# Kernel tuning notes

Hardware: AMD Instinct MI355X
Metric: run time of the kernel (lower is better)

## Reference

```python
import jax, jax.numpy as jnp
import numpy as np

N = 4096
IN_DIM = 256
HID = 64
NHEADS = 4
OUT_DIM = 128
ALPHA = 0.5  # LeakyReLU negative slope
NEG_INF = -9e15


def gat_layer(x, mask, W, a, concat):
    """Dense GraphAttentionLayer (pyGAT style).
    x:[N,Fin], mask:[N,N] bool, W:[Fin,Fout], a:[2*Fout]."""
    Wh = x @ W                                   # [N, Fout]
    Fout = W.shape[1]
    f1 = Wh @ a[:Fout]                           # [N]
    f2 = Wh @ a[Fout:]                           # [N]
    e = jax.nn.leaky_relu(f1[:, None] + f2[None, :], negative_slope=ALPHA)  # [N,N]
    att = jax.nn.softmax(jnp.where(mask, e, NEG_INF), axis=1)               # [N,N]
    h = att @ Wh                                 # [N, Fout]
    return jax.nn.elu(h) if concat else h


def setup_inputs() -> dict:
    key = jax.random.key(0)
    ks = jax.random.split(key, 6)
    x = jax.random.normal(ks[0], (N, IN_DIM), dtype=jnp.float32)
    adj = jax.random.randint(ks[1], (N, N), 0, 2, dtype=jnp.int32)
    s_in = 1.0 / np.sqrt(IN_DIM)
    s_hid = 1.0 / np.sqrt(HID * NHEADS)
    W_heads = jax.random.uniform(ks[2], (NHEADS, IN_DIM, HID), jnp.float32, -s_in, s_in)
    a_heads = jax.random.uniform(ks[3], (NHEADS, 2 * HID), jnp.float32, -s_in, s_in)
    W_out = jax.random.uniform(ks[4], (HID * NHEADS, OUT_DIM), jnp.float32, -s_hid, s_hid)
    a_out = jax.random.uniform(ks[5], (2 * OUT_DIM,), jnp.float32, -s_hid, s_hid)
    return {"x": x, "adj": adj, "W_heads": W_heads, "a_heads": a_heads,
            "W_out": W_out, "a_out": a_out}


def reference(x, adj, W_heads, a_heads, W_out, a_out):
    mask = adj > 0
    # multi-head attention, concat along feature dim
    heads = jax.vmap(lambda W, a: gat_layer(x, mask, W, a, True))(W_heads, a_heads)
    h = jnp.transpose(heads, (1, 0, 2)).reshape(N, NHEADS * HID)  # [N, H*HID]
    # dropout=0 -> identity; final GAT layer (concat=False) + outer ELU
    out = jax.nn.elu(gat_layer(h, mask, W_out, a_out, False))     # [N, OUT_DIM]
    return out
```

## Files before the change

### kernel.cpp

```cpp
#include <hip/hip_runtime.h>
#include <hip/hip_bf16.h>

#define N 4096
#define IN_DIM 256
#define HID 64
#define NHEADS 4
#define OUT_DIM 128
#define LOG2E 1.44269504088896340736f

typedef __attribute__((ext_vector_type(8))) short bf16x8;
typedef __attribute__((ext_vector_type(4))) float f32x4;

__device__ __forceinline__ ushort2 bsplit(float v) {
    const ushort h = __hip_bfloat16_raw(__float2bfloat16(v)).x;
    const float vh = __uint_as_float((unsigned)h << 16);
    const ushort l = __hip_bfloat16_raw(__float2bfloat16(v - vh)).x;
    return make_ushort2(h, l);
}

__global__ __launch_bounds__(256, 4) void prep_kernel(
        const float* __restrict__ x, const float* __restrict__ W,
        const float* __restrict__ a, const int* __restrict__ adj,
        __hip_bfloat16* __restrict__ WhB,
        float* __restrict__ E1, float* __restrict__ S1,
        float* __restrict__ E2, float* __restrict__ S2,
        unsigned* __restrict__ maskT) {
    const int t = threadIdx.x;
    if (blockIdx.x < 256) {
        const int h = t >> 6, lane = t & 63, m = lane & 15, quad = lane >> 4;
        const int i0 = blockIdx.x * 16;
        const float* xrow = x + (size_t)(i0 + m) * IN_DIM;
        const float* Wp = W + (size_t)h * IN_DIM * HID;
        const f32x4 zero = {0.f, 0.f, 0.f, 0.f};
        f32x4 acc[4] = {zero, zero, zero, zero};
        for (int ks = 0; ks < 8; ks++) {
            const int kb = ks * 32 + quad * 8;
            const float4 xa = *(const float4*)(xrow + kb);
            const float4 xb = *(const float4*)(xrow + kb + 4);
            const float xf[8] = {xa.x, xa.y, xa.z, xa.w, xb.x, xb.y, xb.z, xb.w};
            bf16x8 xh, xl;
#pragma unroll
            for (int e = 0; e < 8; e++) {
                const ushort2 s = bsplit(xf[e]);
                xh[e] = (short)s.x; xl[e] = (short)s.y;
            }
#pragma unroll
            for (int ct = 0; ct < 4; ct++) {
                bf16x8 wh, wl;
#pragma unroll
                for (int e = 0; e < 8; e++) {
                    const ushort2 s =
                        bsplit(Wp[(size_t)(kb + e) * HID + ct * 16 + m]);
                    wh[e] = (short)s.x; wl[e] = (short)s.y;
                }
                acc[ct] = __builtin_amdgcn_mfma_f32_16x16x32_bf16(
                    xh, wh, acc[ct], 0, 0, 0);
                acc[ct] = __builtin_amdgcn_mfma_f32_16x16x32_bf16(
                    xl, wh, acc[ct], 0, 0, 0);
                acc[ct] = __builtin_amdgcn_mfma_f32_16x16x32_bf16(
                    xh, wl, acc[ct], 0, 0, 0);
            }
        }
        const int jblk = i0 >> 5, jb2 = (i0 >> 4) & 1;
#pragma unroll
        for (int ct = 0; ct < 4; ct++) {
#pragma unroll
            for (int r = 0; r < 4; r++) {
                const int jo = quad * 4 + r;
                const int lane_idx = m + 16 * (2 * jb2 + (jo >> 3));
                WhB[((((size_t)h * (N / 32) + jblk) * 4 + ct) * 64 + lane_idx) *
                        8 + (jo & 7)] = __float2bfloat16(acc[ct][r]);
            }
        }
        float av1[4], av2[4];
#pragma unroll
        for (int ct = 0; ct < 4; ct++) {
            av1[ct] = a[h * 2 * HID + ct * 16 + m];
            av2[ct] = a[h * 2 * HID + HID + ct * 16 + m];
        }
        float s1[4], s2[4];
#pragma unroll
        for (int r = 0; r < 4; r++) {
            s1[r] = 0.f; s2[r] = 0.f;
#pragma unroll
            for (int ct = 0; ct < 4; ct++) {
                s1[r] += acc[ct][r] * av1[ct];
                s2[r] += acc[ct][r] * av2[ct];
            }
        }
#pragma unroll
        for (int mm = 8; mm > 0; mm >>= 1) {
#pragma unroll
            for (int r = 0; r < 4; r++) {
                s1[r] += __shfl_xor(s1[r], mm, 64);
                s2[r] += __shfl_xor(s2[r], mm, 64);
            }
        }
        if (m == 0) {
#pragma unroll
            for (int r = 0; r < 4; r++) {
                const size_t ix = (size_t)h * N + i0 + quad * 4 + r;
                E1[ix] = __builtin_amdgcn_exp2f(s1[r] * LOG2E);
                S1[ix] = __builtin_amdgcn_exp2f(s1[r] * (0.5f * LOG2E));
                E2[ix] = __builtin_amdgcn_exp2f(s2[r] * LOG2E);
                S2[ix] = __builtin_amdgcn_exp2f(s2[r] * (0.5f * LOG2E));
            }
        }
    } else {
        const int lane = t & 63, w = t >> 6;
        const int i = (blockIdx.x - 256) * 4 + w;
        const int4* arow = (const int4*)(adj + (size_t)i * N);
        for (int jb = 0; jb < N / 256; jb++) {
            const int4 a4 = arow[jb * 64 + lane];
            unsigned long long bal[4];
            bal[0] = __ballot(a4.x > 0);
            bal[1] = __ballot(a4.y > 0);
            bal[2] = __ballot(a4.z > 0);
            bal[3] = __ballot(a4.w > 0);
            if (lane < 8) {
                unsigned word = 0;
#pragma unroll
                for (int e = 0; e < 4; e++) {
                    unsigned xv = (unsigned)(bal[e] >> (8 * lane)) & 0xFFu;
                    xv = (xv | (xv << 12)) & 0x000F000Fu;
                    xv = (xv | (xv << 6))  & 0x03030303u;
                    xv = (xv | (xv << 3))  & 0x11111111u;
                    word |= xv << e;
                }
                maskT[(size_t)(jb * 8 + lane) * N + i] = word;
            }
        }
    }
}

template <int HEADS, int D, int DSL, int G, int MW, int OCC>
__global__ __launch_bounds__(G * 64, OCC) void attn_fused(
        const unsigned* __restrict__ maskT,
        const __hip_bfloat16* __restrict__ WhB,
        const float* __restrict__ E1g, const float* __restrict__ S1g,
        const float* __restrict__ E2g, const float* __restrict__ S2g,
        float* __restrict__ outp) {
    constexpr int CTtot = D / 16;
    constexpr int CTT = CTtot / DSL;
    constexpr int CC = (D == 64) ? 1 : 2;
    constexpr int KSTEPS = N / (32 * G);
    __shared__ float sh[MW * G * 16 * CC * 17];
    __shared__ float dsh[MW * G * 16];
    const int t = threadIdx.x;
    const int g = t >> 6, lane = t & 63;
    const int m = lane & 15, quad = lane >> 4;
    const int h = blockIdx.y / DSL, slc = blockIdx.y % DSL;
    const int i0 = blockIdx.x * (16 * MW);

    float e1v[MW], s1v[MW];
#pragma unroll
    for (int mw = 0; mw < MW; mw++) {
        e1v[mw] = E1g[(size_t)h * N + i0 + mw * 16 + m];
        s1v[mw] = S1g[(size_t)h * N + i0 + mw * 16 + m];
    }

    const unsigned* mp = maskT + (size_t)(g * KSTEPS) * N + i0 + m;
    const float* ep = E2g + (size_t)h * N + g * (N / G) + quad * 8;
    const float* sp = S2g + (size_t)h * N + g * (N / G) + quad * 8;
    const bf16x8* bp = (const bf16x8*)WhB +
                       ((size_t)h * (N / 32) * CTtot +
                        (size_t)(g * KSTEPS) * CTtot + slc * CTT) * 64 + lane;

    const f32x4 zero = {0.f, 0.f, 0.f, 0.f};
    f32x4 acc[MW][CTT];
    f32x4 sac[MW];
#pragma unroll
    for (int mw = 0; mw < MW; mw++) {
        sac[mw] = zero;
#pragma unroll
        for (int ct = 0; ct < CTT; ct++) acc[mw][ct] = zero;
    }
    const short one_bf = (short)0x3F80;
    const bf16x8 ones = {one_bf, one_bf, one_bf, one_bf,
                         one_bf, one_bf, one_bf, one_bf};

    unsigned mwrd[2][MW];
    float4 e2lo[2], e2hi[2], s2lo[2], s2hi[2];
    auto stage = [&](int b) {
#pragma unroll
        for (int mw = 0; mw < MW; mw++) mwrd[b][mw] = mp[mw * 16];
        e2lo[b] = *(const float4*)(ep);
        e2hi[b] = *(const float4*)(ep + 4);
        s2lo[b] = *(const float4*)(sp);
        s2hi[b] = *(const float4*)(sp + 4);
    };

    stage(0); mp += N; ep += 32; sp += 32;
#pragma unroll 2
    for (int ks = 0; ks < KSTEPS; ks++) {
        const int cur = ks & 1;
        bf16x8 bfrag[CTT];
#pragma unroll
        for (int ct = 0; ct < CTT; ct++) bfrag[ct] = bp[ct * 64];
        bp += CTtot * 64;
        if (ks + 1 < KSTEPS) { stage(cur ^ 1); mp += N; ep += 32; sp += 32; }
        const float Ee[8] = {e2lo[cur].x, e2lo[cur].y, e2lo[cur].z, e2lo[cur].w,
                             e2hi[cur].x, e2hi[cur].y, e2hi[cur].z, e2hi[cur].w};
        const float Se[8] = {s2lo[cur].x, s2lo[cur].y, s2lo[cur].z, s2lo[cur].w,
                             s2hi[cur].x, s2hi[cur].y, s2hi[cur].z, s2hi[cur].w};
        bf16x8 afr[MW];
#pragma unroll
        for (int mw = 0; mw < MW; mw++) {
            const unsigned mword = (mwrd[cur][mw] >> (quad * 8)) & 0xFFu;
            const unsigned spread = mword * 0x8001u;
            float p[8];
#pragma unroll
            for (int e = 0; e < 8; e++)
                p[e] = fmaxf(e1v[mw] * Ee[e], s1v[mw] * Se[e]);
            union { bf16x8 v; unsigned u32[4]; __hip_bfloat162 h2[4]; } u;
#pragma unroll
            for (int e2 = 0; e2 < 4; e2++) {
                u.h2[e2] = __float22bfloat162_rn(
                    make_float2(p[2 * e2], p[2 * e2 + 1]));
                const unsigned mk =
                    ((spread >> (2 * e2)) & 0x00010001u) * 0xFFFFu;
                u.u32[e2] &= mk;
            }
            afr[mw] = u.v;
        }
#pragma unroll
        for (int ct = 0; ct < CTT; ct++)
#pragma unroll
            for (int mw = 0; mw < MW; mw++)
                acc[mw][ct] = __builtin_amdgcn_mfma_f32_16x16x32_bf16(
                    afr[mw], bfrag[ct], acc[mw][ct], 0, 0, 0);
#pragma unroll
        for (int mw = 0; mw < MW; mw++)
            sac[mw] = __builtin_amdgcn_mfma_f32_16x16x32_bf16(
                afr[mw], ones, sac[mw], 0, 0, 0);
    }

#pragma unroll
    for (int rd = 0; rd < CTT / CC; rd++) {
#pragma unroll
        for (int mw = 0; mw < MW; mw++) {
#pragma unroll
            for (int cc = 0; cc < CC; cc++) {
#pragma unroll
                for (int r = 0; r < 4; r++)
                    sh[(((mw * G + g) * 16 + quad * 4 + r) * CC + cc) * 17 + m] =
                        acc[mw][rd * CC + cc][r];
            }
            if (rd == 0 && m == 0) {
#pragma unroll
                for (int r = 0; r < 4; r++)
                    dsh[(mw * G + g) * 16 + quad * 4 + r] = sac[mw][r];
            }
        }
        __syncthreads();
        if (t < 16 * CC * 16) {
            int row, chl;
            if (D == 64) { row = t & 15; chl = (t >> 4) & 15; }
            else         { chl = t & 31; row = (t >> 5) & 15; }
#pragma unroll
            for (int mw = 0; mw < MW; mw++) {
                float av = 0.f, ss = 0.f;
#pragma unroll
                for (int gg = 0; gg < G; gg++) {
                    av += sh[(((mw * G + gg) * 16 + row) * CC + (chl >> 4)) * 17 +
                             (chl & 15)];
                    ss += dsh[(mw * G + gg) * 16 + row];
                }
                float v = av / ss;
                v = (v > 0.f) ? v : (__builtin_amdgcn_exp2f(v * LOG2E) - 1.f);
                const int chg = h * D + slc * (CTT * 16) + rd * CC * 16 + chl;
                const int irow = i0 + mw * 16 + row;
                if (D == 64)
                    outp[(size_t)irow * (NHEADS * HID) + chg] = v;
                else
                    outp[(size_t)irow * D + chg] = v;
            }
        }
        __syncthreads();
    }
}

__global__ __launch_bounds__(512, 2) void gemm2_kernel(
        const float* __restrict__ h1, const float* __restrict__ W2,
        const float* __restrict__ a2, __hip_bfloat16* __restrict__ WhB2,
        float* __restrict__ E1, float* __restrict__ S1,
        float* __restrict__ E2, float* __restrict__ S2) {
    __shared__ float fred[8][16][2];
    const int t = threadIdx.x;
    const int w = t >> 6, lane = t & 63, m = lane & 15, quad = lane >> 4;
    const int i0 = blockIdx.x * 16;
    const float* arow = h1 + (size_t)(i0 + m) * IN_DIM;
    const float* wp = W2 + w * 16 + m;
    const f32x4 zero = {0.f, 0.f, 0.f, 0.f};
    f32x4 acc = zero;
    for (int ks = 0; ks < 8; ks++) {
        const int kb = ks * 32 + quad * 8;
        const float4 xa = *(const float4*)(arow + kb);
        const float4 xb = *(const float4*)(arow + kb + 4);
        const float xf[8] = {xa.x, xa.y, xa.z, xa.w, xb.x, xb.y, xb.z, xb.w};
        bf16x8 xh, xl, wh, wl;
#pragma unroll
        for (int e = 0; e < 8; e++) {
            const ushort2 s = bsplit(xf[e]);
            xh[e] = (short)s.x; xl[e] = (short)s.y;
        }
#pragma unroll
        for (int e = 0; e < 8; e++) {
            const ushort2 s = bsplit(wp[(size_t)(kb + e) * OUT_DIM]);
            wh[e] = (short)s.x; wl[e] = (short)s.y;
        }
        acc = __builtin_amdgcn_mfma_f32_16x16x32_bf16(xh, wh, acc, 0, 0, 0);
        acc = __builtin_amdgcn_mfma_f32_16x16x32_bf16(xl, wh, acc, 0, 0, 0);
        acc = __builtin_amdgcn_mfma_f32_16x16x32_bf16(xh, wl, acc, 0, 0, 0);
    }
    const int jblk = i0 >> 5, jb2 = (i0 >> 4) & 1;
#pragma unroll
    for (int r = 0; r < 4; r++) {
        const int jo = quad * 4 + r;
        const int lane_idx = m + 16 * (2 * jb2 + (jo >> 3));
        WhB2[(((size_t)jblk * 8 + w) * 64 + lane_idx) * 8 + (jo & 7)] =
            __float2bfloat16(acc[r]);
    }
    const float av1 = a2[w * 16 + m], av2 = a2[OUT_DIM + w * 16 + m];
    float s1[4], s2[4];
#pragma unroll
    for (int r = 0; r < 4; r++) { s1[r] = acc[r] * av1; s2[r] = acc[r] * av2; }
#pragma unroll
    for (int mm = 8; mm > 0; mm >>= 1) {
#pragma unroll
        for (int r = 0; r < 4; r++) {
            s1[r] += __shfl_xor(s1[r], mm, 64);
            s2[r] += __shfl_xor(s2[r], mm, 64);
        }
    }
    if (m == 0) {
#pragma unroll
        for (int r = 0; r < 4; r++) {
            fred[w][quad * 4 + r][0] = s1[r];
            fred[w][quad * 4 + r][1] = s2[r];
        }
    }
    __syncthreads();
    if (t < 32) {
        const int row = t & 15, fn = t >> 4;
        float s = 0.f;
#pragma unroll
        for (int w8 = 0; w8 < 8; w8++) s += fred[w8][row][fn];
        const float e = __builtin_amdgcn_exp2f(s * LOG2E);
        const float sq = __builtin_amdgcn_exp2f(s * (0.5f * LOG2E));
        if (fn) { E2[i0 + row] = e; S2[i0 + row] = sq; }
        else    { E1[i0 + row] = e; S1[i0 + row] = sq; }
    }
}

extern "C" void kernel_launch(void* const* d_in, const int* in_sizes, int n_in,
                              void* d_out, int out_size, void* d_ws, size_t ws_size,
                              hipStream_t stream) {
    const float* x   = (const float*)d_in[0];
    const int*   adj = (const int*)d_in[1];
    const float* Wh_ = (const float*)d_in[2];
    const float* ah  = (const float*)d_in[3];
    const float* W2  = (const float*)d_in[4];
    const float* a2  = (const float*)d_in[5];
    float* out = (float*)d_out;

    float* ws = (float*)d_ws;
    float* E1a = ws;
    float* S1a = E1a + (size_t)NHEADS * N;
    float* E2a = S1a + (size_t)NHEADS * N;
    float* S2a = E2a + (size_t)NHEADS * N;
    float* E1b = S2a + (size_t)NHEADS * N;
    float* S1b = E1b + N;
    float* E2b = S1b + N;
    float* S2b = E2b + N;
    float* h1  = S2b + N;
    __hip_bfloat16* WhB1 = (__hip_bfloat16*)(h1 + (size_t)IN_DIM * N);
    __hip_bfloat16* WhB2 = WhB1 + (size_t)NHEADS * HID * N;
    unsigned* maskT = (unsigned*)(WhB2 + (size_t)OUT_DIM * N);

    prep_kernel<<<1280, 256, 0, stream>>>(x, Wh_, ah, adj, WhB1,
                                          E1a, S1a, E2a, S2a, maskT);
    attn_fused<NHEADS, HID, 1, 8, 2, 2>
        <<<dim3(N / 32, NHEADS), 512, 0, stream>>>(maskT, WhB1,
                                                   E1a, S1a, E2a, S2a, h1);
    gemm2_kernel<<<N / 16, 512, 0, stream>>>(h1, W2, a2, WhB2,
                                             E1b, S1b, E2b, S2b);
    attn_fused<1, OUT_DIM, 1, 8, 1, 2>
        <<<dim3(N / 16, 1), 512, 0, stream>>>(maskT, WhB2,
                                              E1b, S1b, E2b, S2b, out);
}
```

Measured before the change: 168.7 us.

## Fuse four kernels into one persistent megakernel with software grid barriers

Merges prep, first attention, second GEMM and final attention into a single persistent kernel of 512 blocks, separated by atomic-counter grid barriers. A memset resets the barrier counters before each launch. The goal is to drop three kernel launch gaps and the tail idle time between stages. In exchange, correctness now relies on all 512 blocks being co-resident, and the spin barriers use a timeout break. The second attention stage also changes its tiling from one block per 16 rows with a full 128-column slice to two 64-column slices, so it fits the fixed grid.

```diff
diff --git a/kernel.cpp b/kernel.cpp
--- a/kernel.cpp
+++ b/kernel.cpp
@@ -7,6 +7,7 @@
 #define NHEADS 4
 #define OUT_DIM 128
 #define LOG2E 1.44269504088896340736f
+#define NBLK 512
 
 typedef __attribute__((ext_vector_type(8))) short bf16x8;
 typedef __attribute__((ext_vector_type(4))) float f32x4;
@@ -18,97 +19,188 @@
     return make_ushort2(h, l);
 }
 
-__global__ __launch_bounds__(256, 4) void prep_kernel(
+__device__ __forceinline__ void grid_sync(unsigned* cnt) {
+    __syncthreads();
+    if (threadIdx.x == 0) {
+        __threadfence();
+        __hip_atomic_fetch_add(cnt, 1u, __ATOMIC_RELAXED,
+                               __HIP_MEMORY_SCOPE_AGENT);
+        int spins = 0;
+        while (__hip_atomic_load(cnt, __ATOMIC_RELAXED,
+                                 __HIP_MEMORY_SCOPE_AGENT) < NBLK) {
+            __builtin_amdgcn_s_sleep(8);
+            if (++spins > (1 << 22)) break;
+        }
+        __threadfence();
+    }
+    __syncthreads();
+}
+
+template <int D, int DSL, int G, int MW>
+__device__ __forceinline__ void attn_stage(
+        const int bx, const int by,
+        const unsigned* __restrict__ maskT,
+        const __hip_bfloat16* __restrict__ WhB,
+        const float* __restrict__ E1g, const float* __restrict__ S1g,
+        const float* __restrict__ E2g, const float* __restrict__ S2g,
+        float* __restrict__ outp, float* __restrict__ sh,
+        float* __restrict__ dsh) {
+    constexpr int CTtot = D / 16;
+    constexpr int CTT = CTtot / DSL;
+    constexpr int CC = (D == 64) ? 1 : 2;
+    constexpr int KSTEPS = N / (32 * G);
+    const int t = threadIdx.x;
+    const int g = t >> 6, lane = t & 63;
+    const int m = lane & 15, quad = lane >> 4;
+    const int h = by / DSL, slc = by % DSL;
+    const int i0 = bx * (16 * MW);
+
+    float e1v[MW], s1v[MW];
+#pragma unroll
+    for (int mw = 0; mw < MW; mw++) {
+        e1v[mw] = E1g[(size_t)h * N + i0 + mw * 16 + m];
+        s1v[mw] = S1g[(size_t)h * N + i0 + mw * 16 + m];
+    }
+    const unsigned* mp = maskT + (size_t)(g * KSTEPS) * N + i0 + m;
+    const float* ep = E2g + (size_t)h * N + g * (N / G) + quad * 8;
+    const float* sp = S2g + (size_t)h * N + g * (N / G) + quad * 8;
+    const bf16x8* bp = (const bf16x8*)WhB +
+                       ((size_t)h * (N / 32) * CTtot +
+                        (size_t)(g * KSTEPS) * CTtot + slc * CTT) * 64 + lane;
+
+    const f32x4 zero = {0.f, 0.f, 0.f, 0.f};
+    f32x4 acc[MW][CTT];
+    f32x4 sac[MW];
+#pragma unroll
+    for (int mw = 0; mw < MW; mw++) {
+        sac[mw] = zero;
+#pragma unroll
+        for (int ct = 0; ct < CTT; ct++) acc[mw][ct] = zero;
+    }
+    const short one_bf = (short)0x3F80;
+    const bf16x8 ones = {one_bf, one_bf, one_bf, one_bf,
+                         one_bf, one_bf, one_bf, one_bf};
+
+    unsigned mwrd[2][MW];
+    float4 e2lo[2], e2hi[2], s2lo[2], s2hi[2];
+    auto stage = [&](int b) {
+#pragma unroll
+        for (int mw = 0; mw < MW; mw++) mwrd[b][mw] = mp[mw * 16];
+        e2lo[b] = *(const float4*)(ep);
+        e2hi[b] = *(const float4*)(ep + 4);
+        s2lo[b] = *(const float4*)(sp);
+        s2hi[b] = *(const float4*)(sp + 4);
+    };
+
+    stage(0); mp += N; ep += 32; sp += 32;
+#pragma unroll 2
+    for (int ks = 0; ks < KSTEPS; ks++) {
+        const int cur = ks & 1;
+        bf16x8 bfrag[CTT];
+#pragma unroll
+        for (int ct = 0; ct < CTT; ct++) bfrag[ct] = bp[ct * 64];
+        bp += CTtot * 64;
+        if (ks + 1 < KSTEPS) { stage(cur ^ 1); mp += N; ep += 32; sp += 32; }
+        const float Ee[8] = {e2lo[cur].x, e2lo[cur].y, e2lo[cur].z, e2lo[cur].w,
+                             e2hi[cur].x, e2hi[cur].y, e2hi[cur].z, e2hi[cur].w};
+        const float Se[8] = {s2lo[cur].x, s2lo[cur].y, s2lo[cur].z, s2lo[cur].w,
+                             s2hi[cur].x, s2hi[cur].y, s2hi[cur].z, s2hi[cur].w};
+        bf16x8 afr[MW];
+#pragma unroll
+        for (int mw = 0; mw < MW; mw++) {
+            const unsigned mword = (mwrd[cur][mw] >> (quad * 8)) & 0xFFu;
+            const unsigned spread = mword * 0x8001u;
+            float p[8];
+#pragma unroll
+            for (int e = 0; e < 8; e++)
+                p[e] = fmaxf(e1v[mw] * Ee[e], s1v[mw] * Se[e]);
+            union { bf16x8 v; unsigned u32[4]; __hip_bfloat162 h2[4]; } u;
+#pragma unroll
+            for (int e2 = 0; e2 < 4; e2++) {
+                u.h2[e2] = __float22bfloat162_rn(
+                    make_float2(p[2 * e2], p[2 * e2 + 1]));
+                const unsigned mk =
+                    ((spread >> (2 * e2)) & 0x00010001u) * 0xFFFFu;
+                u.u32[e2] &= mk;
+            }
+            afr[mw] = u.v;
+        }
+#pragma unroll
+        for (int ct = 0; ct < CTT; ct++)
+#pragma unroll
+            for (int mw = 0; mw < MW; mw++)
+                acc[mw][ct] = __builtin_amdgcn_mfma_f32_16x16x32_bf16(
+                    afr[mw], bfrag[ct], acc[mw][ct], 0, 0, 0);
+#pragma unroll
+        for (int mw = 0; mw < MW; mw++)
+            sac[mw] = __builtin_amdgcn_mfma_f32_16x16x32_bf16(
+                afr[mw], ones, sac[mw], 0, 0, 0);
+    }
+
+#pragma unroll
+    for (int rd = 0; rd < CTT / CC; rd++) {
+#pragma unroll
+        for (int mw = 0; mw < MW; mw++) {
+#pragma unroll
+            for (int cc = 0; cc < CC; cc++) {
+#pragma unroll
+                for (int r = 0; r < 4; r++)
+                    sh[(((mw * G + g) * 16 + quad * 4 + r) * CC + cc) * 17 + m] =
+                        acc[mw][rd * CC + cc][r];
+            }
+            if (rd == 0 && m == 0) {
+#pragma unroll
+                for (int r = 0; r < 4; r++)
+                    dsh[(mw * G + g) * 16 + quad * 4 + r] = sac[mw][r];
+            }
+        }
+        __syncthreads();
+        if (t < 16 * CC * 16) {
+            int row, chl;
+            if (D == 64) { row = t & 15; chl = (t >> 4) & 15; }
+            else         { chl = t & 31; row = (t >> 5) & 15; }
+#pragma unroll
+            for (int mw = 0; mw < MW; mw++) {
+                float av = 0.f, ss = 0.f;
+#pragma unroll
+                for (int gg = 0; gg < G; gg++) {
+                    av += sh[(((mw * G + gg) * 16 + row) * CC + (chl >> 4)) * 17 +
+                             (chl & 15)];
+                    ss += dsh[(mw * G + gg) * 16 + row];
+                }
+                float v = av / ss;
+                v = (v > 0.f) ? v : (__builtin_amdgcn_exp2f(v * LOG2E) - 1.f);
+                const int chg = h * D + slc * (CTT * 16) + rd * CC * 16 + chl;
+                const int irow = i0 + mw * 16 + row;
+                if (D == 64)
+                    outp[(size_t)irow * (NHEADS * HID) + chg] = v;
+                else
+                    outp[(size_t)irow * D + chg] = v;
+            }
+        }
+        __syncthreads();
+    }
+}
+
+__global__ __launch_bounds__(512, 4) void mega(
         const float* __restrict__ x, const float* __restrict__ W,
         const float* __restrict__ a, const int* __restrict__ adj,
-        __hip_bfloat16* __restrict__ WhB,
-        float* __restrict__ E1, float* __restrict__ S1,
-        float* __restrict__ E2, float* __restrict__ S2,
-        unsigned* __restrict__ maskT) {
+        const float* __restrict__ W2, const float* __restrict__ a2,
+        __hip_bfloat16* __restrict__ WhB1, __hip_bfloat16* __restrict__ WhB2,
+        float* __restrict__ E1a, float* __restrict__ S1a,
+        float* __restrict__ E2a, float* __restrict__ S2a,
+        float* __restrict__ E1b, float* __restrict__ S1b,
+        float* __restrict__ E2b, float* __restrict__ S2b,
+        float* __restrict__ h1, unsigned* __restrict__ maskT,
+        float* __restrict__ out, unsigned* __restrict__ bars) {
+    __shared__ float shbuf[4608];
+    __shared__ float dshbuf[256];
     const int t = threadIdx.x;
-    if (blockIdx.x < 256) {
-        const int h = t >> 6, lane = t & 63, m = lane & 15, quad = lane >> 4;
-        const int i0 = blockIdx.x * 16;
-        const float* xrow = x + (size_t)(i0 + m) * IN_DIM;
-        const float* Wp = W + (size_t)h * IN_DIM * HID;
-        const f32x4 zero = {0.f, 0.f, 0.f, 0.f};
-        f32x4 acc[4] = {zero, zero, zero, zero};
-        for (int ks = 0; ks < 8; ks++) {
-            const int kb = ks * 32 + quad * 8;
-            const float4 xa = *(const float4*)(xrow + kb);
-            const float4 xb = *(const float4*)(xrow + kb + 4);
-            const float xf[8] = {xa.x, xa.y, xa.z, xa.w, xb.x, xb.y, xb.z, xb.w};
-            bf16x8 xh, xl;
-#pragma unroll
-            for (int e = 0; e < 8; e++) {
-                const ushort2 s = bsplit(xf[e]);
-                xh[e] = (short)s.x; xl[e] = (short)s.y;
-            }
-#pragma unroll
-            for (int ct = 0; ct < 4; ct++) {
-                bf16x8 wh, wl;
-#pragma unroll
-                for (int e = 0; e < 8; e++) {
-                    const ushort2 s =
-                        bsplit(Wp[(size_t)(kb + e) * HID + ct * 16 + m]);
-                    wh[e] = (short)s.x; wl[e] = (short)s.y;
-                }
-                acc[ct] = __builtin_amdgcn_mfma_f32_16x16x32_bf16(
-                    xh, wh, acc[ct], 0, 0, 0);
-                acc[ct] = __builtin_amdgcn_mfma_f32_16x16x32_bf16(
-                    xl, wh, acc[ct], 0, 0, 0);
-                acc[ct] = __builtin_amdgcn_mfma_f32_16x16x32_bf16(
-                    xh, wl, acc[ct], 0, 0, 0);
-            }
-        }
-        const int jblk = i0 >> 5, jb2 = (i0 >> 4) & 1;
-#pragma unroll
-        for (int ct = 0; ct < 4; ct++) {
-#pragma unroll
-            for (int r = 0; r < 4; r++) {
-                const int jo = quad * 4 + r;
-                const int lane_idx = m + 16 * (2 * jb2 + (jo >> 3));
-                WhB[((((size_t)h * (N / 32) + jblk) * 4 + ct) * 64 + lane_idx) *
-                        8 + (jo & 7)] = __float2bfloat16(acc[ct][r]);
-            }
-        }
-        float av1[4], av2[4];
-#pragma unroll
-        for (int ct = 0; ct < 4; ct++) {
-            av1[ct] = a[h * 2 * HID + ct * 16 + m];
-            av2[ct] = a[h * 2 * HID + HID + ct * 16 + m];
-        }
-        float s1[4], s2[4];
-#pragma unroll
-        for (int r = 0; r < 4; r++) {
-            s1[r] = 0.f; s2[r] = 0.f;
-#pragma unroll
-            for (int ct = 0; ct < 4; ct++) {
-                s1[r] += acc[ct][r] * av1[ct];
-                s2[r] += acc[ct][r] * av2[ct];
-            }
-        }
-#pragma unroll
-        for (int mm = 8; mm > 0; mm >>= 1) {
-#pragma unroll
-            for (int r = 0; r < 4; r++) {
-                s1[r] += __shfl_xor(s1[r], mm, 64);
-                s2[r] += __shfl_xor(s2[r], mm, 64);
-            }
-        }
-        if (m == 0) {
-#pragma unroll
-            for (int r = 0; r < 4; r++) {
-                const size_t ix = (size_t)h * N + i0 + quad * 4 + r;
-                E1[ix] = __builtin_amdgcn_exp2f(s1[r] * LOG2E);
-                S1[ix] = __builtin_amdgcn_exp2f(s1[r] * (0.5f * LOG2E));
-                E2[ix] = __builtin_amdgcn_exp2f(s2[r] * LOG2E);
-                S2[ix] = __builtin_amdgcn_exp2f(s2[r] * (0.5f * LOG2E));
-            }
-        }
-    } else {
-        const int lane = t & 63, w = t >> 6;
-        const int i = (blockIdx.x - 256) * 4 + w;
+    const int bid = blockIdx.x;
+    const int w = t >> 6, lane = t & 63;
+
+    {
+        const int i = bid * 8 + w;
         const int4* arow = (const int4*)(adj + (size_t)i * N);
         for (int jb = 0; jb < N / 256; jb++) {
             const int4 a4 = arow[jb * 64 + lane];
@@ -130,227 +222,166 @@
                 maskT[(size_t)(jb * 8 + lane) * N + i] = word;
             }
         }
-    }
-}
-
-template <int HEADS, int D, int DSL, int G, int MW, int OCC>
-__global__ __launch_bounds__(G * 64, OCC) void attn_fused(
-        const unsigned* __restrict__ maskT,
-        const __hip_bfloat16* __restrict__ WhB,
-        const float* __restrict__ E1g, const float* __restrict__ S1g,
-        const float* __restrict__ E2g, const float* __restrict__ S2g,
-        float* __restrict__ outp) {
-    constexpr int CTtot = D / 16;
-    constexpr int CTT = CTtot / DSL;
-    constexpr int CC = (D == 64) ? 1 : 2;
-    constexpr int KSTEPS = N / (32 * G);
-    __shared__ float sh[MW * G * 16 * CC * 17];
-    __shared__ float dsh[MW * G * 16];
-    const int t = threadIdx.x;
-    const int g = t >> 6, lane = t & 63;
-    const int m = lane & 15, quad = lane >> 4;
-    const int h = blockIdx.y / DSL, slc = blockIdx.y % DSL;
-    const int i0 = blockIdx.x * (16 * MW);
-
-    float e1v[MW], s1v[MW];
-#pragma unroll
-    for (int mw = 0; mw < MW; mw++) {
-        e1v[mw] = E1g[(size_t)h * N + i0 + mw * 16 + m];
-        s1v[mw] = S1g[(size_t)h * N + i0 + mw * 16 + m];
-    }
-
-    const unsigned* mp = maskT + (size_t)(g * KSTEPS) * N + i0 + m;
-    const float* ep = E2g + (size_t)h * N + g * (N / G) + quad * 8;
-    const float* sp = S2g + (size_t)h * N + g * (N / G) + quad * 8;
-    const bf16x8* bp = (const bf16x8*)WhB +
-                       ((size_t)h * (N / 32) * CTtot +
-                        (size_t)(g * KSTEPS) * CTtot + slc * CTT) * 64 + lane;
-
-    const f32x4 zero = {0.f, 0.f, 0.f, 0.f};
-    f32x4 acc[MW][CTT];
-    f32x4 sac[MW];
-#pragma unroll
-    for (int mw = 0; mw < MW; mw++) {
-        sac[mw] = zero;
-#pragma unroll
-        for (int ct = 0; ct < CTT; ct++) acc[mw][ct] = zero;
-    }
-    const short one_bf = (short)0x3F80;
-    const bf16x8 ones = {one_bf, one_bf, one_bf, one_bf,
-                         one_bf, one_bf, one_bf, one_bf};
-
-    unsigned mwrd[2][MW];
-    float4 e2lo[2], e2hi[2], s2lo[2], s2hi[2];
-    auto stage = [&](int b) {
-#pragma unroll
-        for (int mw = 0; mw < MW; mw++) mwrd[b][mw] = mp[mw * 16];
-        e2lo[b] = *(const float4*)(ep);
-        e2hi[b] = *(const float4*)(ep + 4);
-        s2lo[b] = *(const float4*)(sp);
-        s2hi[b] = *(const float4*)(sp + 4);
-    };
-
-    stage(0); mp += N; ep += 32; sp += 32;
-#pragma unroll 2
-    for (int ks = 0; ks < KSTEPS; ks++) {
-        const int cur = ks & 1;
-        bf16x8 bfrag[CTT];
-#pragma unroll
-        for (int ct = 0; ct < CTT; ct++) bfrag[ct] = bp[ct * 64];
-        bp += CTtot * 64;
-        if (ks + 1 < KSTEPS) { stage(cur ^ 1); mp += N; ep += 32; sp += 32; }
-        const float Ee[8] = {e2lo[cur].x, e2lo[cur].y, e2lo[cur].z, e2lo[cur].w,
-                             e2hi[cur].x, e2hi[cur].y, e2hi[cur].z, e2hi[cur].w};
-        const float Se[8] = {s2lo[cur].x, s2lo[cur].y, s2lo[cur].z, s2lo[cur].w,
-                             s2hi[cur].x, s2hi[cur].y, s2hi[cur].z, s2hi[cur].w};
-        bf16x8 afr[MW];
-#pragma unroll
-        for (int mw = 0; mw < MW; mw++) {
-            const unsigned mword = (mwrd[cur][mw] >> (quad * 8)) & 0xFFu;
-            const unsigned spread = mword * 0x8001u;
-            float p[8];
-#pragma unroll
-            for (int e = 0; e < 8; e++)
-                p[e] = fmaxf(e1v[mw] * Ee[e], s1v[mw] * Se[e]);
-            union { bf16x8 v; unsigned u32[4]; __hip_bfloat162 h2[4]; } u;
-#pragma unroll
-            for (int e2 = 0; e2 < 4; e2++) {
-                u.h2[e2] = __float22bfloat162_rn(
-                    make_float2(p[2 * e2], p[2 * e2 + 1]));
-                const unsigned mk =
-                    ((spread >> (2 * e2)) & 0x00010001u) * 0xFFFFu;
-                u.u32[e2] &= mk;
-            }
-            afr[mw] = u.v;
-        }
-#pragma unroll
-        for (int ct = 0; ct < CTT; ct++)
-#pragma unroll
-            for (int mw = 0; mw < MW; mw++)
-                acc[mw][ct] = __builtin_amdgcn_mfma_f32_16x16x32_bf16(
-                    afr[mw], bfrag[ct], acc[mw][ct], 0, 0, 0);
-#pragma unroll
-        for (int mw = 0; mw < MW; mw++)
-            sac[mw] = __builtin_amdgcn_mfma_f32_16x16x32_bf16(
-                afr[mw], ones, sac[mw], 0, 0, 0);
-    }
-
-#pragma unroll
-    for (int rd = 0; rd < CTT / CC; rd++) {
-#pragma unroll
-        for (int mw = 0; mw < MW; mw++) {
-#pragma unroll
-            for (int cc = 0; cc < CC; cc++) {
-#pragma unroll
-                for (int r = 0; r < 4; r++)
-                    sh[(((mw * G + g) * 16 + quad * 4 + r) * CC + cc) * 17 + m] =
-                        acc[mw][rd * CC + cc][r];
-            }
-            if (rd == 0 && m == 0) {
-#pragma unroll
-                for (int r = 0; r < 4; r++)
-                    dsh[(mw * G + g) * 16 + quad * 4 + r] = sac[mw][r];
+        if (w < 2) {
+            const int h = (bid & 1) * 2 + w;
+            const int m = lane & 15, quad = lane >> 4;
+            const int i0 = (bid >> 1) * 16;
+            const float* xrow = x + (size_t)(i0 + m) * IN_DIM;
+            const float* Wp = W + (size_t)h * IN_DIM * HID;
+            const f32x4 zero = {0.f, 0.f, 0.f, 0.f};
+            f32x4 acc[4] = {zero, zero, zero, zero};
+            for (int ks = 0; ks < 8; ks++) {
+                const int kb = ks * 32 + quad * 8;
+                const float4 xa = *(const float4*)(xrow + kb);
+                const float4 xb = *(const float4*)(xrow + kb + 4);
+                const float xf[8] = {xa.x, xa.y, xa.z, xa.w,
+                                     xb.x, xb.y, xb.z, xb.w};
+                bf16x8 xh, xl;
+#pragma unroll
+                for (int e = 0; e < 8; e++) {
+                    const ushort2 s = bsplit(xf[e]);
+                    xh[e] = (short)s.x; xl[e] = (short)s.y;
+                }
+#pragma unroll
+                for (int ct = 0; ct < 4; ct++) {
+                    bf16x8 wh, wl;
+#pragma unroll
+                    for (int e = 0; e < 8; e++) {
+                        const ushort2 s =
+                            bsplit(Wp[(size_t)(kb + e) * HID + ct * 16 + m]);
+                        wh[e] = (short)s.x; wl[e] = (short)s.y;
+                    }
+                    acc[ct] = __builtin_amdgcn_mfma_f32_16x16x32_bf16(
+                        xh, wh, acc[ct], 0, 0, 0);
+                    acc[ct] = __builtin_amdgcn_mfma_f32_16x16x32_bf16(
+                        xl, wh, acc[ct], 0, 0, 0);
+                    acc[ct] = __builtin_amdgcn_mfma_f32_16x16x32_bf16(
+                        xh, wl, acc[ct], 0, 0, 0);
+                }
+            }
+            const int jblk = i0 >> 5, jb2 = (i0 >> 4) & 1;
+#pragma unroll
+            for (int ct = 0; ct < 4; ct++) {
+#pragma unroll
+                for (int r = 0; r < 4; r++) {
+                    const int jo = quad * 4 + r;
+                    const int lane_idx = m + 16 * (2 * jb2 + (jo >> 3));
+                    WhB1[((((size_t)h * (N / 32) + jblk) * 4 + ct) * 64 +
+                          lane_idx) * 8 + (jo & 7)] = __float2bfloat16(acc[ct][r]);
+                }
+            }
+            float av1[4], av2[4];
+#pragma unroll
+            for (int ct = 0; ct < 4; ct++) {
+                av1[ct] = a[h * 2 * HID + ct * 16 + m];
+                av2[ct] = a[h * 2 * HID + HID + ct * 16 + m];
+            }
+            float s1[4], s2[4];
+#pragma unroll
+            for (int r = 0; r < 4; r++) {
+                s1[r] = 0.f; s2[r] = 0.f;
+#pragma unroll
+                for (int ct = 0; ct < 4; ct++) {
+                    s1[r] += acc[ct][r] * av1[ct];
+                    s2[r] += acc[ct][r] * av2[ct];
+                }
+            }
+#pragma unroll
+            for (int mm = 8; mm > 0; mm >>= 1) {
+#pragma unroll
+                for (int r = 0; r < 4; r++) {
+                    s1[r] += __shfl_xor(s1[r], mm, 64);
+                    s2[r] += __shfl_xor(s2[r], mm, 64);
+                }
+            }
+            if (m == 0) {
+#pragma unroll
+                for (int r = 0; r < 4; r++) {
+                    const size_t ix = (size_t)h * N + i0 + quad * 4 + r;
+                    E1a[ix] = __builtin_amdgcn_exp2f(s1[r] * LOG2E);
+                    S1a[ix] = __builtin_amdgcn_exp2f(s1[r] * (0.5f * LOG2E));
+                    E2a[ix] = __builtin_amdgcn_exp2f(s2[r] * LOG2E);
+                    S2a[ix] = __builtin_amdgcn_exp2f(s2[r] * (0.5f * LOG2E));
+                }
+            }
+        }
+    }
+    grid_sync(bars + 0);
+
+    attn_stage<HID, 1, 8, 2>(bid & 127, bid >> 7, maskT, WhB1,
+                             E1a, S1a, E2a, S2a, h1, shbuf, dshbuf);
+    grid_sync(bars + 1);
+
+    if (bid < 256) {
+        const int m = lane & 15, quad = lane >> 4;
+        const int i0 = bid * 16;
+        const float* arow = h1 + (size_t)(i0 + m) * IN_DIM;
+        const float* wp = W2 + w * 16 + m;
+        const f32x4 zero = {0.f, 0.f, 0.f, 0.f};
+        f32x4 acc = zero;
+        for (int ks = 0; ks < 8; ks++) {
+            const int kb = ks * 32 + quad * 8;
+            const float4 xa = *(const float4*)(arow + kb);
+            const float4 xb = *(const float4*)(arow + kb + 4);
+            const float xf[8] = {xa.x, xa.y, xa.z, xa.w, xb.x, xb.y, xb.z, xb.w};
+            bf16x8 xh, xl, wh, wl;
+#pragma unroll
+            for (int e = 0; e < 8; e++) {
+                const ushort2 s = bsplit(xf[e]);
+                xh[e] = (short)s.x; xl[e] = (short)s.y;
+            }
+#pragma unroll
+            for (int e = 0; e < 8; e++) {
+                const ushort2 s = bsplit(wp[(size_t)(kb + e) * OUT_DIM]);
+                wh[e] = (short)s.x; wl[e] = (short)s.y;
+            }
+            acc = __builtin_amdgcn_mfma_f32_16x16x32_bf16(xh, wh, acc, 0, 0, 0);
+            acc = __builtin_amdgcn_mfma_f32_16x16x32_bf16(xl, wh, acc, 0, 0, 0);
+            acc = __builtin_amdgcn_mfma_f32_16x16x32_bf16(xh, wl, acc, 0, 0, 0);
+        }
+        const int jblk = i0 >> 5, jb2 = (i0 >> 4) & 1;
+#pragma unroll
+        for (int r = 0; r < 4; r++) {
+            const int jo = quad * 4 + r;
+            const int lane_idx = m + 16 * (2 * jb2 + (jo >> 3));
+            WhB2[(((size_t)jblk * 8 + w) * 64 + lane_idx) * 8 + (jo & 7)] =
+                __float2bfloat16(acc[r]);
+        }
+        const float av1 = a2[w * 16 + m], av2 = a2[OUT_DIM + w * 16 + m];
+        float s1[4], s2[4];
+#pragma unroll
+        for (int r = 0; r < 4; r++) { s1[r] = acc[r] * av1; s2[r] = acc[r] * av2; }
+#pragma unroll
+        for (int mm = 8; mm > 0; mm >>= 1) {
+#pragma unroll
+            for (int r = 0; r < 4; r++) {
+                s1[r] += __shfl_xor(s1[r], mm, 64);
+                s2[r] += __shfl_xor(s2[r], mm, 64);
+            }
+        }
+        if (m == 0) {
+#pragma unroll
+            for (int r = 0; r < 4; r++) {
+                dshbuf[((w * 16) + quad * 4 + r) * 2 + 0] = s1[r];
+                dshbuf[((w * 16) + quad * 4 + r) * 2 + 1] = s2[r];
             }
         }
         __syncthreads();
-        if (t < 16 * CC * 16) {
-            int row, chl;
-            if (D == 64) { row = t & 15; chl = (t >> 4) & 15; }
-            else         { chl = t & 31; row = (t >> 5) & 15; }
-#pragma unroll
-            for (int mw = 0; mw < MW; mw++) {
-                float av = 0.f, ss = 0.f;
-#pragma unroll
-                for (int gg = 0; gg < G; gg++) {
-                    av += sh[(((mw * G + gg) * 16 + row) * CC + (chl >> 4)) * 17 +
-                             (chl & 15)];
-                    ss += dsh[(mw * G + gg) * 16 + row];
-                }
-                float v = av / ss;
-                v = (v > 0.f) ? v : (__builtin_amdgcn_exp2f(v * LOG2E) - 1.f);
-                const int chg = h * D + slc * (CTT * 16) + rd * CC * 16 + chl;
-                const int irow = i0 + mw * 16 + row;
-                if (D == 64)
-                    outp[(size_t)irow * (NHEADS * HID) + chg] = v;
-                else
-                    outp[(size_t)irow * D + chg] = v;
-            }
-        }
-        __syncthreads();
-    }
-}
-
-__global__ __launch_bounds__(512, 2) void gemm2_kernel(
-        const float* __restrict__ h1, const float* __restrict__ W2,
-        const float* __restrict__ a2, __hip_bfloat16* __restrict__ WhB2,
-        float* __restrict__ E1, float* __restrict__ S1,
-        float* __restrict__ E2, float* __restrict__ S2) {
-    __shared__ float fred[8][16][2];
-    const int t = threadIdx.x;
-    const int w = t >> 6, lane = t & 63, m = lane & 15, quad = lane >> 4;
-    const int i0 = blockIdx.x * 16;
-    const float* arow = h1 + (size_t)(i0 + m) * IN_DIM;
-    const float* wp = W2 + w * 16 + m;
-    const f32x4 zero = {0.f, 0.f, 0.f, 0.f};
-    f32x4 acc = zero;
-    for (int ks = 0; ks < 8; ks++) {
-        const int kb = ks * 32 + quad * 8;
-        const float4 xa = *(const float4*)(arow + kb);
-        const float4 xb = *(const float4*)(arow + kb + 4);
-        const float xf[8] = {xa.x, xa.y, xa.z, xa.w, xb.x, xb.y, xb.z, xb.w};
-        bf16x8 xh, xl, wh, wl;
-#pragma unroll
-        for (int e = 0; e < 8; e++) {
-            const ushort2 s = bsplit(xf[e]);
-            xh[e] = (short)s.x; xl[e] = (short)s.y;
-        }
-#pragma unroll
-        for (int e = 0; e < 8; e++) {
-            const ushort2 s = bsplit(wp[(size_t)(kb + e) * OUT_DIM]);
-            wh[e] = (short)s.x; wl[e] = (short)s.y;
-        }
-        acc = __builtin_amdgcn_mfma_f32_16x16x32_bf16(xh, wh, acc, 0, 0, 0);
-        acc = __builtin_amdgcn_mfma_f32_16x16x32_bf16(xl, wh, acc, 0, 0, 0);
-        acc = __builtin_amdgcn_mfma_f32_16x16x32_bf16(xh, wl, acc, 0, 0, 0);
-    }
-    const int jblk = i0 >> 5, jb2 = (i0 >> 4) & 1;
-#pragma unroll
-    for (int r = 0; r < 4; r++) {
-        const int jo = quad * 4 + r;
-        const int lane_idx = m + 16 * (2 * jb2 + (jo >> 3));
-        WhB2[(((size_t)jblk * 8 + w) * 64 + lane_idx) * 8 + (jo & 7)] =
-            __float2bfloat16(acc[r]);
-    }
-    const float av1 = a2[w * 16 + m], av2 = a2[OUT_DIM + w * 16 + m];
-    float s1[4], s2[4];
-#pragma unroll
-    for (int r = 0; r < 4; r++) { s1[r] = acc[r] * av1; s2[r] = acc[r] * av2; }
-#pragma unroll
-    for (int mm = 8; mm > 0; mm >>= 1) {
-#pragma unroll
-        for (int r = 0; r < 4; r++) {
-            s1[r] += __shfl_xor(s1[r], mm, 64);
-            s2[r] += __shfl_xor(s2[r], mm, 64);
-        }
-    }
-    if (m == 0) {
-#pragma unroll
-        for (int r = 0; r < 4; r++) {
-            fred[w][quad * 4 + r][0] = s1[r];
-            fred[w][quad * 4 + r][1] = s2[r];
-        }
-    }
-    __syncthreads();
-    if (t < 32) {
-        const int row = t & 15, fn = t >> 4;
-        float s = 0.f;
-#pragma unroll
-        for (int w8 = 0; w8 < 8; w8++) s += fred[w8][row][fn];
-        const float e = __builtin_amdgcn_exp2f(s * LOG2E);
-        const float sq = __builtin_amdgcn_exp2f(s * (0.5f * LOG2E));
-        if (fn) { E2[i0 + row] = e; S2[i0 + row] = sq; }
-        else    { E1[i0 + row] = e; S1[i0 + row] = sq; }
-    }
+        if (t < 32) {
+            const int row = t & 15, fn = t >> 4;
+            float s = 0.f;
+#pragma unroll
+            for (int w8 = 0; w8 < 8; w8++) s += dshbuf[(w8 * 16 + row) * 2 + fn];
+            const float e = __builtin_amdgcn_exp2f(s * LOG2E);
+            const float sq = __builtin_amdgcn_exp2f(s * (0.5f * LOG2E));
+            if (fn) { E2b[i0 + row] = e; S2b[i0 + row] = sq; }
+            else    { E1b[i0 + row] = e; S1b[i0 + row] = sq; }
+        }
+    }
+    grid_sync(bars + 2);
+
+    attn_stage<OUT_DIM, 2, 8, 1>(bid & 255, bid >> 8, maskT, WhB2,
+                                 E1b, S1b, E2b, S2b, out, shbuf, dshbuf);
 }
 
 extern "C" void kernel_launch(void* const* d_in, const int* in_sizes, int n_in,
@@ -377,15 +408,10 @@
     __hip_bfloat16* WhB1 = (__hip_bfloat16*)(h1 + (size_t)IN_DIM * N);
     __hip_bfloat16* WhB2 = WhB1 + (size_t)NHEADS * HID * N;
     unsigned* maskT = (unsigned*)(WhB2 + (size_t)OUT_DIM * N);
-
-    prep_kernel<<<1280, 256, 0, stream>>>(x, Wh_, ah, adj, WhB1,
-                                          E1a, S1a, E2a, S2a, maskT);
-    attn_fused<NHEADS, HID, 1, 8, 2, 2>
-        <<<dim3(N / 32, NHEADS), 512, 0, stream>>>(maskT, WhB1,
-                                                   E1a, S1a, E2a, S2a, h1);
-    gemm2_kernel<<<N / 16, 512, 0, stream>>>(h1, W2, a2, WhB2,
-                                             E1b, S1b, E2b, S2b);
-    attn_fused<1, OUT_DIM, 1, 8, 1, 2>
-        <<<dim3(N / 16, 1), 512, 0, stream>>>(maskT, WhB2,
-                                              E1b, S1b, E2b, S2b, out);
+    unsigned* bars = maskT + (size_t)(N / 32) * N;
+
+    hipMemsetAsync(bars, 0, 3 * sizeof(unsigned), stream);
+    mega<<<NBLK, 512, 0, stream>>>(x, Wh_, ah, adj, W2, a2, WhB1, WhB2,
+                                   E1a, S1a, E2a, S2a, E1b, S1b, E2b, S2b,
+                                   h1, maskT, out, bars);
 }
```

After: 320.4 us. 89.9% more time.
